# Optimization experiments

Hardware: AMD Instinct MI355X
Metric: run time of the kernel (lower is better)

The kernel has to match this reference:

```python
import jax, jax.numpy as jnp
import numpy as np

N = 131072      # number of RoIs (instances)
D = 1024        # in_channels
H = 1024        # hidden dim (hard-coded in module)
L = 4           # number of FPN levels / routed experts
STD = 0.01      # init std for all weights (biases zero)


def setup_inputs() -> dict:
    key = jax.random.key(0)
    k = jax.random.split(key, 5)
    x = jax.random.normal(k[0], (N, D), dtype=jnp.float32)
    levels = jax.random.randint(k[1], (N,), 0, L, dtype=jnp.int32)
    # Per-level MLP params, normal(std=0.01) weights, zero biases.
    W1 = jax.random.normal(k[2], (L, D, H), dtype=jnp.float32) * STD
    b1 = jnp.zeros((L, H), dtype=jnp.float32)
    W2 = jax.random.normal(k[3], (L, H, H), dtype=jnp.float32) * STD
    b2 = jnp.zeros((L, H), dtype=jnp.float32)
    W3 = jax.random.normal(k[4], (L, H, 1), dtype=jnp.float32) * STD
    b3 = jnp.zeros((L, 1), dtype=jnp.float32)
    return {"x": x, "levels": levels, "W1": W1, "b1": b1,
            "W2": W2, "b2": b2, "W3": W3, "b3": b3}


def reference(x, levels, W1, b1, W2, b2, W3, b3):
    # Hard-routed per-level 3-layer MLP (FC-ReLU x2 + FC), dropout in eval
    # mode (identity). Rows routed to level l get that level's MLP output;
    # implemented jit-compatibly with a fixed loop over the 4 levels and a
    # row mask instead of data-dependent gather/scatter.
    result = jnp.zeros((x.shape[0], 1), dtype=x.dtype)
    for lvl in range(L):
        h = jax.nn.relu(x @ W1[lvl] + b1[lvl])       # [N, H]
        h = jax.nn.relu(h @ W2[lvl] + b2[lvl])       # [N, H]
        out = h @ W3[lvl] + b3[lvl]                  # [N, 1]
        result = jnp.where((levels == lvl)[:, None], out, result)
    return result
```

## Files before the change

### kernel.cpp

```cpp
#include <hip/hip_runtime.h>

#define NROWS   131072
#define KDIM    1024
#define NLVL    4
#define SLOT_CAP 132096
#define NSB     516
#define NNB     8

#define OFF_IDX  1024ull
#define OFF_PART (OFF_IDX + (size_t)SLOT_CAP * 4)
#define OFF_WT1  (OFF_PART + (size_t)SLOT_CAP * 64)
#define OFF_WT2  (OFF_WT1 + 8388608ull)
#define OFF_XBF  (OFF_WT2 + 8388608ull)
#define OFF_H1   (OFF_XBF + 268435456ull)

typedef __bf16 bf16x8 __attribute__((ext_vector_type(8)));
typedef float f32x4 __attribute__((ext_vector_type(4)));
typedef unsigned short u16x4 __attribute__((ext_vector_type(4)));

__device__ __forceinline__ unsigned short f2bf(float f) {
  unsigned int u = __float_as_uint(f);
  u += 0x7fffu + ((u >> 16) & 1u);
  return (unsigned short)(u >> 16);
}

__device__ __forceinline__ void gld_lds16(const void* g, void* l) {
  __builtin_amdgcn_global_load_lds(
      (const __attribute__((address_space(1))) void*)g,
      (__attribute__((address_space(3))) void*)l, 16, 0, 0);
}


__global__ void k_hist(const int* __restrict__ levels, int n, int* __restrict__ meta) {
  __shared__ int h[NLVL];
  if (threadIdx.x < NLVL) h[threadIdx.x] = 0;
  __syncthreads();
  for (int t = blockIdx.x * blockDim.x + threadIdx.x; t < n; t += gridDim.x * blockDim.x)
    atomicAdd(&h[levels[t]], 1);
  __syncthreads();
  if (threadIdx.x < NLVL) atomicAdd(&meta[threadIdx.x], h[threadIdx.x]);
}

__global__ void k_seg(int* meta) {
  if (threadIdx.x == 0 && blockIdx.x == 0) {
    int s = 0;
    for (int l = 0; l < NLVL; ++l) {
      int pc = (meta[l] + 255) & ~255;
      meta[8 + l] = s;
      meta[12 + l] = pc;
      s += pc;
    }
  }
}

__global__ void k_scatter(const int* __restrict__ levels, int n,
                          int* __restrict__ meta, int* __restrict__ idx) {
  __shared__ int h[NLVL], base[NLVL], cur[NLVL];
  int t = blockIdx.x * blockDim.x + threadIdx.x;
  if (threadIdx.x < NLVL) { h[threadIdx.x] = 0; cur[threadIdx.x] = 0; }
  __syncthreads();
  int lvl = 0;
  if (t < n) { lvl = levels[t]; atomicAdd(&h[lvl], 1); }
  __syncthreads();
  if (threadIdx.x < NLVL)
    base[threadIdx.x] = atomicAdd(&meta[4 + threadIdx.x], h[threadIdx.x]);
  __syncthreads();
  if (t < n) {
    int p = atomicAdd(&cur[lvl], 1);
    idx[meta[8 + lvl] + base[lvl] + p] = t;
  }
}

__global__ void k_cvt_x(const f32x4* __restrict__ x, u16x4* __restrict__ xb, int n4) {
  for (int t = blockIdx.x * blockDim.x + threadIdx.x; t < n4; t += gridDim.x * blockDim.x) {
    f32x4 v = x[t];
    u16x4 o;
    o[0] = f2bf(v[0]); o[1] = f2bf(v[1]); o[2] = f2bf(v[2]); o[3] = f2bf(v[3]);
    xb[t] = o;
  }
}

__global__ void k_twt(const float* __restrict__ W, unsigned short* __restrict__ Wt) {
  __shared__ float tile[32][33];
  int lvl = blockIdx.z;
  int k0 = blockIdx.x * 32, n0 = blockIdx.y * 32;
  int tx = threadIdx.x, ty = threadIdx.y;
  const float* Wp = W + (size_t)lvl * 1048576;
  unsigned short* Wtp = Wt + (size_t)lvl * 1048576;
#pragma unroll
  for (int i = 0; i < 4; ++i)
    tile[ty + i * 8][tx] = Wp[(size_t)(k0 + ty + i * 8) * 1024 + n0 + tx];
  __syncthreads();
#pragma unroll
  for (int i = 0; i < 4; ++i) {
    int nn = ty + i * 8;
    Wtp[(size_t)(n0 + nn) * 1024 + k0 + tx] = f2bf(tile[tx][nn]);
  }
}

#define BARRM   asm volatile("s_barrier" ::: "memory")
#define WAIT_L  asm volatile("s_waitcnt lgkmcnt(0)" ::: "memory")
#define WAIT_V9 asm volatile("s_waitcnt vmcnt(9)" ::: "memory")
#define WAIT_V6 asm volatile("s_waitcnt vmcnt(6)" ::: "memory")
#define WAIT_V3 asm volatile("s_waitcnt vmcnt(3)" ::: "memory")
#define WAIT_V0 asm volatile("s_waitcnt vmcnt(0)" ::: "memory")
#define PRIO(x) __builtin_amdgcn_s_setprio(x)

#define RDW(p,kk) { const char* p_ = lds + (p)*49152 + 32768 + (kk)*8192 + offW; \
  wf[0] = *(const bf16x8*)(p_);        wf[1] = *(const bf16x8*)(p_ + 1024);     \
  wf[2] = *(const bf16x8*)(p_ + 2048); wf[3] = *(const bf16x8*)(p_ + 3072); }
#define RDX(p,kk) { const char* p_ = lds + (p)*49152 + (kk)*16384 + offX;       \
  xf[0] = *(const bf16x8*)(p_);        xf[1] = *(const bf16x8*)(p_ + 1024);     \
  xf[2] = *(const bf16x8*)(p_ + 2048); xf[3] = *(const bf16x8*)(p_ + 3072); }
#define MMA4 { _Pragma("unroll") for (int nf_ = 0; nf_ < 4; ++nf_) { \
  _Pragma("unroll") for (int mf_ = 0; mf_ < 4; ++mf_) \
    acc[nf_][mf_] = __builtin_amdgcn_mfma_f32_16x16x32_bf16(wf[nf_], xf[mf_], acc[nf_][mf_], 0, 0, 0); } }
#define STGW(p,t,kk) gld_lds16(ws0 + (t)*128 + (kk)*64, \
  (char*)lds + (p)*49152 + 32768 + (kk)*8192 + (w << 10))
#define STGX(p,t,kk) { char* d_ = (char*)lds + (p)*49152 + (kk)*16384 + (w << 10); \
  gld_lds16(xs0 + (t)*128 + (kk)*64, d_); \
  gld_lds16(xs1 + (t)*128 + (kk)*64, d_ + 8192); }

template <int PASS>
__global__ __launch_bounds__(512, 2) void k_gemm(
    const unsigned short* __restrict__ Asrc,
    const unsigned short* __restrict__ Wt,
    const float* __restrict__ bias,
    const float* __restrict__ w3,
    const int* __restrict__ meta,
    const int* __restrict__ idx,
    unsigned short* __restrict__ hout,
    float* __restrict__ partial) {
  __shared__ __align__(16) char lds[147456];

  const int bid = blockIdx.x;
  const int swz = (bid & 7) * NSB + (bid >> 3);
  const int nb = swz & 7;
  const int sb = swz >> 3;
  const int slotbase = sb * 256;
  if (slotbase >= meta[11] + meta[15]) return;
  int lvl;
  if      (slotbase < meta[9])  lvl = 0;
  else if (slotbase < meta[10]) lvl = 1;
  else if (slotbase < meta[11]) lvl = 2;
  else                          lvl = 3;

  const int tid = threadIdx.x;
  const int ln  = tid & 63;
  const int w   = tid >> 6;
  const int wm  = w & 3;
  const int wn  = w >> 2;
  const int l15 = ln & 15;

  const int srow = w * 16 + (ln >> 2);
  const int cch  = (ln & 3) ^ ((srow >> 1) & 3);
  int ar0, ar1;
  if (PASS == 1) { ar0 = idx[slotbase + srow]; ar1 = idx[slotbase + srow + 128]; }
  else           { ar0 = slotbase + srow;      ar1 = slotbase + srow + 128; }
  const char* xs0 = (const char*)Asrc + (size_t)ar0 * 2048 + cch * 16;
  const char* xs1 = (const char*)Asrc + (size_t)ar1 * 2048 + cch * 16;
  const char* ws0 = (const char*)Wt + ((size_t)lvl << 21)
                    + (size_t)(nb * 128 + srow) * 2048 + cch * 16;

  const int xorc = ((ln >> 4) ^ ((l15 >> 1) & 3)) * 16;
  const int offX = wm * 4096 + l15 * 64 + xorc;
  const int offW = wn * 4096 + l15 * 64 + xorc;

  const f32x4 vzero = {0.f, 0.f, 0.f, 0.f};
  f32x4 acc[4][4];
#pragma unroll
  for (int a = 0; a < 4; ++a)
#pragma unroll
    for (int b = 0; b < 4; ++b) acc[a][b] = vzero;
  bf16x8 wf[4], xf[4];

  STGW(0, 0, 0); STGX(0, 0, 0); STGW(0, 0, 1); STGX(0, 0, 1);
  STGW(1, 1, 0); STGX(1, 1, 0); STGW(1, 1, 1); STGX(1, 1, 1);
  WAIT_V6;
  BARRM;

#pragma unroll
  for (int t = 0; t < 14; ++t) {
    const int p  = t % 3;
    const int ps = (t + 2) % 3;
    RDW(p, 0); RDX(p, 0);
    STGW(ps, t + 2, 0); STGX(ps, t + 2, 0);
    BARRM; WAIT_L; PRIO(1); MMA4; PRIO(0); WAIT_V9; BARRM;
    RDW(p, 1); RDX(p, 1);
    STGW(ps, t + 2, 1); STGX(ps, t + 2, 1);
    BARRM; WAIT_L; PRIO(1); MMA4; PRIO(0); WAIT_V9; BARRM;
  }

  RDW(2, 0); RDX(2, 0);
  BARRM; WAIT_L; PRIO(1); MMA4; PRIO(0); WAIT_V6; BARRM;
  RDW(2, 1); RDX(2, 1);
  BARRM; WAIT_L; PRIO(1); MMA4; PRIO(0); WAIT_V3; BARRM;
  RDW(0, 0); RDX(0, 0);
  BARRM; WAIT_L; PRIO(1); MMA4; PRIO(0); WAIT_V0; BARRM;
  RDW(0, 1); RDX(0, 1);
  WAIT_L; PRIO(1); MMA4; PRIO(0);

  const float* bv = bias + lvl * 1024;
  const int n_lo = (ln >> 4) * 4;

  if (PASS == 1) {
#pragma unroll
    for (int nf = 0; nf < 4; ++nf) {
#pragma unroll
      for (int mf = 0; mf < 4; ++mf) {
        int slot = slotbase + wm * 64 + mf * 16 + l15;
        int col = nb * 128 + wn * 64 + nf * 16 + n_lo;
        f32x4 bb = *(const f32x4*)&bv[col];
        f32x4 v = acc[nf][mf];
        u16x4 o;
#pragma unroll
        for (int r = 0; r < 4; ++r) o[r] = f2bf(fmaxf(v[r] + bb[r], 0.f));
        *(u16x4*)&hout[(size_t)slot * 1024 + col] = o;
      }
    }
  } else {
    const float* w3v = w3 + lvl * 1024;
    float ps4[4] = {0.f, 0.f, 0.f, 0.f};
#pragma unroll
    for (int mf = 0; mf < 4; ++mf) {
#pragma unroll
      for (int nf = 0; nf < 4; ++nf) {
        int col = nb * 128 + wn * 64 + nf * 16 + n_lo;
        f32x4 bb = *(const f32x4*)&bv[col];
        f32x4 ww = *(const f32x4*)&w3v[col];
        f32x4 v = acc[nf][mf];
#pragma unroll
        for (int r = 0; r < 4; ++r) ps4[mf] += fmaxf(v[r] + bb[r], 0.f) * ww[r];
      }
    }
#pragma unroll
    for (int mf = 0; mf < 4; ++mf) {
      float p = ps4[mf];
      p += __shfl_xor(p, 16);
      p += __shfl_xor(p, 32);
      if (ln < 16) {
        int slot = slotbase + wm * 64 + mf * 16 + ln;
        partial[(size_t)slot * 16 + nb * 2 + wn] = p;
      }
    }
  }
}

__global__ void k_final(const int* __restrict__ meta, const int* __restrict__ idx,
                        const float* __restrict__ partial, const float* __restrict__ b3,
                        float* __restrict__ out) {
  int t = blockIdx.x * blockDim.x + threadIdx.x;
  int total = meta[11] + meta[15];
  if (t >= total) return;
  int lvl;
  if (t < meta[9]) lvl = 0;
  else if (t < meta[10]) lvl = 1;
  else if (t < meta[11]) lvl = 2;
  else lvl = 3;
  int local = t - meta[8 + lvl];
  if (local >= meta[lvl]) return;
  int row = idx[t];
  const float* pp = partial + (size_t)t * 16;
  float s = 0.f;
#pragma unroll
  for (int j = 0; j < 16; ++j) s += pp[j];
  out[row] = s + b3[lvl];
}

extern "C" void kernel_launch(void* const* d_in, const int* in_sizes, int n_in,
                              void* d_out, int out_size, void* d_ws, size_t ws_size,
                              hipStream_t stream) {
  const float* x      = (const float*)d_in[0];
  const int*   levels = (const int*)d_in[1];
  const float* W1     = (const float*)d_in[2];
  const float* b1     = (const float*)d_in[3];
  const float* W2     = (const float*)d_in[4];
  const float* b2     = (const float*)d_in[5];
  const float* W3     = (const float*)d_in[6];
  const float* b3     = (const float*)d_in[7];
  float* out = (float*)d_out;

  char* ws = (char*)d_ws;
  int* meta = (int*)ws;
  int* idx = (int*)(ws + OFF_IDX);
  float* partial = (float*)(ws + OFF_PART);
  unsigned short* Wt1 = (unsigned short*)(ws + OFF_WT1);
  unsigned short* Wt2 = (unsigned short*)(ws + OFF_WT2);
  unsigned short* xb  = (unsigned short*)(ws + OFF_XBF);
  unsigned short* h1  = (unsigned short*)(ws + OFF_H1);

  hipMemsetAsync(d_ws, 0, OFF_IDX + (size_t)SLOT_CAP * 4, stream);
  k_hist<<<256, 256, 0, stream>>>(levels, NROWS, meta);
  k_seg<<<1, 64, 0, stream>>>(meta);
  k_scatter<<<512, 256, 0, stream>>>(levels, NROWS, meta, idx);
  k_cvt_x<<<2048, 256, 0, stream>>>((const f32x4*)x, (u16x4*)xb, NROWS * (KDIM / 4));
  k_twt<<<dim3(32, 32, 4), dim3(32, 8), 0, stream>>>(W1, Wt1);
  k_twt<<<dim3(32, 32, 4), dim3(32, 8), 0, stream>>>(W2, Wt2);

  k_gemm<1><<<NSB * NNB, 512, 0, stream>>>(xb, Wt1, b1, nullptr, meta, idx, h1, nullptr);
  k_gemm<2><<<NSB * NNB, 512, 0, stream>>>(h1, Wt2, b2, W3, meta, idx, nullptr, partial);

  k_final<<<516, 256, 0, stream>>>(meta, idx, partial, b3, out);
}
```

Before: 958.6 us.

## Widen GEMM tile to 256x256 with 1024-thread blocks and 32-wide K steps

Changes the grouped GEMM blocks from 256x128 output tiles with 512 threads to 256x256 tiles with 1024 threads (16 waves), halving the number of N-blocks. The K step per pipeline stage shrinks from 64 to 32, with a 3-stage LDS ring of 32KB per stage and a new swizzle pattern. The goal is more reuse of each staged A tile across output columns, which cuts global/L2 traffic for the gathered activations. In exchange, more loop iterations and barriers are needed, each barrier now spans more waves, and occupancy per CU is likely lower.

After: 829.8 us. -13.4%, faster.

```diff
diff --git a/kernel.cpp b/kernel.cpp
--- a/kernel.cpp
+++ b/kernel.cpp
@@ -5,7 +5,7 @@
 #define NLVL    4
 #define SLOT_CAP 132096
 #define NSB     516
-#define NNB     8
+#define NNB     4
 
 #define OFF_IDX  1024ull
 #define OFF_PART (OFF_IDX + (size_t)SLOT_CAP * 4)
@@ -100,29 +100,25 @@
 
 #define BARRM   asm volatile("s_barrier" ::: "memory")
 #define WAIT_L  asm volatile("s_waitcnt lgkmcnt(0)" ::: "memory")
-#define WAIT_V9 asm volatile("s_waitcnt vmcnt(9)" ::: "memory")
-#define WAIT_V6 asm volatile("s_waitcnt vmcnt(6)" ::: "memory")
-#define WAIT_V3 asm volatile("s_waitcnt vmcnt(3)" ::: "memory")
+#define WAIT_V2 asm volatile("s_waitcnt vmcnt(2)" ::: "memory")
 #define WAIT_V0 asm volatile("s_waitcnt vmcnt(0)" ::: "memory")
 #define PRIO(x) __builtin_amdgcn_s_setprio(x)
 
-#define RDW(p,kk) { const char* p_ = lds + (p)*49152 + 32768 + (kk)*8192 + offW; \
+#define RDW(p) { const char* p_ = lds + (p)*32768 + offW; \
   wf[0] = *(const bf16x8*)(p_);        wf[1] = *(const bf16x8*)(p_ + 1024);     \
   wf[2] = *(const bf16x8*)(p_ + 2048); wf[3] = *(const bf16x8*)(p_ + 3072); }
-#define RDX(p,kk) { const char* p_ = lds + (p)*49152 + (kk)*16384 + offX;       \
+#define RDX(p) { const char* p_ = lds + (p)*32768 + offX;       \
   xf[0] = *(const bf16x8*)(p_);        xf[1] = *(const bf16x8*)(p_ + 1024);     \
   xf[2] = *(const bf16x8*)(p_ + 2048); xf[3] = *(const bf16x8*)(p_ + 3072); }
 #define MMA4 { _Pragma("unroll") for (int nf_ = 0; nf_ < 4; ++nf_) { \
   _Pragma("unroll") for (int mf_ = 0; mf_ < 4; ++mf_) \
     acc[nf_][mf_] = __builtin_amdgcn_mfma_f32_16x16x32_bf16(wf[nf_], xf[mf_], acc[nf_][mf_], 0, 0, 0); } }
-#define STGW(p,t,kk) gld_lds16(ws0 + (t)*128 + (kk)*64, \
-  (char*)lds + (p)*49152 + 32768 + (kk)*8192 + (w << 10))
-#define STGX(p,t,kk) { char* d_ = (char*)lds + (p)*49152 + (kk)*16384 + (w << 10); \
-  gld_lds16(xs0 + (t)*128 + (kk)*64, d_); \
-  gld_lds16(xs1 + (t)*128 + (kk)*64, d_ + 8192); }
+#define STG(p,t) { char* b_ = (char*)lds + (p)*32768 + (w << 10); \
+  gld_lds16(xs0 + (t)*64, b_); \
+  gld_lds16(ws0 + (t)*64, b_ + 16384); }
 
 template <int PASS>
-__global__ __launch_bounds__(512, 2) void k_gemm(
+__global__ __launch_bounds__(1024, 4) void k_gemm(
     const unsigned short* __restrict__ Asrc,
     const unsigned short* __restrict__ Wt,
     const float* __restrict__ bias,
@@ -131,12 +127,12 @@
     const int* __restrict__ idx,
     unsigned short* __restrict__ hout,
     float* __restrict__ partial) {
-  __shared__ __align__(16) char lds[147456];
+  __shared__ __align__(16) char lds[98304];
 
   const int bid = blockIdx.x;
-  const int swz = (bid & 7) * NSB + (bid >> 3);
-  const int nb = swz & 7;
-  const int sb = swz >> 3;
+  const int swz = (bid & 7) * (NSB * NNB / 8) + (bid >> 3);
+  const int nb = swz & 3;
+  const int sb = swz >> 2;
   const int slotbase = sb * 256;
   if (slotbase >= meta[11] + meta[15]) return;
   int lvl;
@@ -153,18 +149,17 @@
   const int l15 = ln & 15;
 
   const int srow = w * 16 + (ln >> 2);
-  const int cch  = (ln & 3) ^ ((srow >> 1) & 3);
-  int ar0, ar1;
-  if (PASS == 1) { ar0 = idx[slotbase + srow]; ar1 = idx[slotbase + srow + 128]; }
-  else           { ar0 = slotbase + srow;      ar1 = slotbase + srow + 128; }
+  const int cch  = (ln & 3) ^ ((ln >> 3) & 3);
+  int ar0;
+  if (PASS == 1) ar0 = idx[slotbase + srow];
+  else           ar0 = slotbase + srow;
   const char* xs0 = (const char*)Asrc + (size_t)ar0 * 2048 + cch * 16;
-  const char* xs1 = (const char*)Asrc + (size_t)ar1 * 2048 + cch * 16;
   const char* ws0 = (const char*)Wt + ((size_t)lvl << 21)
-                    + (size_t)(nb * 128 + srow) * 2048 + cch * 16;
+                    + (size_t)(nb * 256 + srow) * 2048 + cch * 16;
 
   const int xorc = ((ln >> 4) ^ ((l15 >> 1) & 3)) * 16;
-  const int offX = wm * 4096 + l15 * 64 + xorc;
-  const int offW = wn * 4096 + l15 * 64 + xorc;
+  const int offX = (wm * 64 + l15) * 64 + xorc;
+  const int offW = 16384 + (wn * 64 + l15) * 64 + xorc;
 
   const f32x4 vzero = {0.f, 0.f, 0.f, 0.f};
   f32x4 acc[4][4];
@@ -174,30 +169,22 @@
     for (int b = 0; b < 4; ++b) acc[a][b] = vzero;
   bf16x8 wf[4], xf[4];
 
-  STGW(0, 0, 0); STGX(0, 0, 0); STGW(0, 0, 1); STGX(0, 0, 1);
-  STGW(1, 1, 0); STGX(1, 1, 0); STGW(1, 1, 1); STGX(1, 1, 1);
-  WAIT_V6;
+  STG(0, 0); STG(1, 1);
+  WAIT_V2;
   BARRM;
 
 #pragma unroll
-  for (int t = 0; t < 14; ++t) {
+  for (int t = 0; t < 30; ++t) {
     const int p  = t % 3;
     const int ps = (t + 2) % 3;
-    RDW(p, 0); RDX(p, 0);
-    STGW(ps, t + 2, 0); STGX(ps, t + 2, 0);
-    BARRM; WAIT_L; PRIO(1); MMA4; PRIO(0); WAIT_V9; BARRM;
-    RDW(p, 1); RDX(p, 1);
-    STGW(ps, t + 2, 1); STGX(ps, t + 2, 1);
-    BARRM; WAIT_L; PRIO(1); MMA4; PRIO(0); WAIT_V9; BARRM;
-  }
-
-  RDW(2, 0); RDX(2, 0);
-  BARRM; WAIT_L; PRIO(1); MMA4; PRIO(0); WAIT_V6; BARRM;
-  RDW(2, 1); RDX(2, 1);
-  BARRM; WAIT_L; PRIO(1); MMA4; PRIO(0); WAIT_V3; BARRM;
-  RDW(0, 0); RDX(0, 0);
+    RDW(p); RDX(p);
+    STG(ps, t + 2);
+    BARRM; WAIT_L; PRIO(1); MMA4; PRIO(0); WAIT_V2; BARRM;
+  }
+
+  RDW(0); RDX(0);
   BARRM; WAIT_L; PRIO(1); MMA4; PRIO(0); WAIT_V0; BARRM;
-  RDW(0, 1); RDX(0, 1);
+  RDW(1); RDX(1);
   WAIT_L; PRIO(1); MMA4; PRIO(0);
 
   const float* bv = bias + lvl * 1024;
@@ -209,7 +196,7 @@
 #pragma unroll
       for (int mf = 0; mf < 4; ++mf) {
         int slot = slotbase + wm * 64 + mf * 16 + l15;
-        int col = nb * 128 + wn * 64 + nf * 16 + n_lo;
+        int col = nb * 256 + wn * 64 + nf * 16 + n_lo;
         f32x4 bb = *(const f32x4*)&bv[col];
         f32x4 v = acc[nf][mf];
         u16x4 o;
@@ -225,7 +212,7 @@
     for (int mf = 0; mf < 4; ++mf) {
 #pragma unroll
       for (int nf = 0; nf < 4; ++nf) {
-        int col = nb * 128 + wn * 64 + nf * 16 + n_lo;
+        int col = nb * 256 + wn * 64 + nf * 16 + n_lo;
         f32x4 bb = *(const f32x4*)&bv[col];
         f32x4 ww = *(const f32x4*)&w3v[col];
         f32x4 v = acc[nf][mf];
@@ -240,7 +227,7 @@
       p += __shfl_xor(p, 32);
       if (ln < 16) {
         int slot = slotbase + wm * 64 + mf * 16 + ln;
-        partial[(size_t)slot * 16 + nb * 2 + wn] = p;
+        partial[(size_t)slot * 16 + nb * 4 + wn] = p;
       }
     }
   }
@@ -297,8 +284,8 @@
   k_twt<<<dim3(32, 32, 4), dim3(32, 8), 0, stream>>>(W1, Wt1);
   k_twt<<<dim3(32, 32, 4), dim3(32, 8), 0, stream>>>(W2, Wt2);
 
-  k_gemm<1><<<NSB * NNB, 512, 0, stream>>>(xb, Wt1, b1, nullptr, meta, idx, h1, nullptr);
-  k_gemm<2><<<NSB * NNB, 512, 0, stream>>>(h1, Wt2, b2, W3, meta, idx, nullptr, partial);
+  k_gemm<1><<<NSB * NNB, 1024, 0, stream>>>(xb, Wt1, b1, nullptr, meta, idx, h1, nullptr);
+  k_gemm<2><<<NSB * NNB, 1024, 0, stream>>>(h1, Wt2, b2, W3, meta, idx, nullptr, partial);
 
   k_final<<<516, 256, 0, stream>>>(meta, idx, partial, b3, out);
 }
```
